# Optimization experiments

Measured on AMD Instinct MI355X. Metric: run time of the kernel, lower is better.

Reference implementation:

```python
import jax, jax.numpy as jnp
import numpy as np

ITERATIONS = 100
TEMP = 1.0
EPS = 0.001


def setup_inputs() -> dict:
    key = jax.random.key(0)
    x = jax.random.normal(key, (16, 512, 512), dtype=jnp.float32)
    return {"x": x}


def reference(x):
    # exp(x / temp) + eps, then 100 alternating row/col normalizations
    y = jnp.exp(x / TEMP) + EPS

    def step(y, _):
        y = y / jnp.sum(y, axis=-1, keepdims=True)  # row normalize
        y = y / jnp.sum(y, axis=-2, keepdims=True)  # column normalize
        return y, None

    y, _ = jax.lax.scan(step, y, None, length=ITERATIONS)
    return y
```

## Files before the change

kernel.cpp:

```cpp
#include <hip/hip_runtime.h>
#include <hip/hip_bf16.h>


#define BATCH   16
#define NDIM    512
#define NNEL    (NDIM * NDIM)
#define ITERS   100
#define EPS_K   0.001f
#define WPB     16
#define RPW     32
#define THREADS 512
#define CSTRIDE 64

__device__ __forceinline__ unsigned short f2bf(float f) {
  unsigned int u = __float_as_uint(f);
  u += 0x7fffu + ((u >> 16) & 1u);
  return (unsigned short)(u >> 16);
}

__global__ __launch_bounds__(256) void prep_kernel(const float* __restrict__ x,
                                                   unsigned short* __restrict__ mh,
                                                   unsigned short* __restrict__ mht,
                                                   int* __restrict__ counters) {
  __shared__ float t[64][65];
  const int bid = blockIdx.x;
  if (bid == 0 && threadIdx.x < 32) counters[(int)threadIdx.x * CSTRIDE] = 0;
  const int b    = bid >> 6;
  const int tile = bid & 63;
  const int tr   = (tile >> 3) << 6;
  const int tc   = (tile & 7) << 6;
  const int lx   = threadIdx.x & 63;
  const int ty   = threadIdx.x >> 6;
  const size_t base = (size_t)b * NNEL;
#pragma unroll
  for (int k = 0; k < 16; ++k) {
    int row = (k << 2) + ty;
    float v = expf(x[base + (size_t)(tr + row) * NDIM + tc + lx]) + EPS_K;
    mh[base + (size_t)(tr + row) * NDIM + tc + lx] = f2bf(v);
    t[row][lx] = v;
  }
  __syncthreads();
#pragma unroll
  for (int k = 0; k < 16; ++k) {
    int row = (k << 2) + ty;
    mht[base + (size_t)(tc + row) * NDIM + tr + lx] = f2bf(t[lx][row]);
  }
}

__device__ __forceinline__ void wg_barrier(int* cnt, int target) {
  __syncthreads();
  if (threadIdx.x == 0) {
    __hip_atomic_fetch_add(cnt, 1, __ATOMIC_RELEASE, __HIP_MEMORY_SCOPE_AGENT);
    int guard = 0;
    while (__hip_atomic_load(cnt, __ATOMIC_RELAXED, __HIP_MEMORY_SCOPE_AGENT) < target) {
      __builtin_amdgcn_s_sleep(2);
      if (++guard > (1 << 22)) break;
    }
    asm volatile("" ::: "memory");
  }
  __syncthreads();
}

__device__ __forceinline__ float dot_row(const unsigned short* mrow, int lane,
                                         const float* cc) {
  uint4 v = *(const uint4*)(mrow + lane * 8);
  float p;
  p  = __uint_as_float(v.x << 16)         * cc[0];
  p += __uint_as_float(v.x & 0xffff0000u) * cc[1];
  p += __uint_as_float(v.y << 16)         * cc[2];
  p += __uint_as_float(v.y & 0xffff0000u) * cc[3];
  p += __uint_as_float(v.z << 16)         * cc[4];
  p += __uint_as_float(v.z & 0xffff0000u) * cc[5];
  p += __uint_as_float(v.w << 16)         * cc[6];
  p += __uint_as_float(v.w & 0xffff0000u) * cc[7];
#pragma unroll
  for (int o = 32; o > 0; o >>= 1) p += __shfl_xor(p, o, 64);
  return p;
}

__global__ __launch_bounds__(THREADS, 4) void sinkhorn_kernel(
    const unsigned short* mh, const unsigned short* mht, float* yout,
    float* r_g, float* c_g, int* counters) {
  __shared__ alignas(16) float vec[NDIM];
  __shared__ float rown[RPW];
  __shared__ alignas(16) unsigned short stage[RPW * NDIM];
  const int wg   = blockIdx.x;
  const int b    = wg >> 4;
  const int sub  = wg & 15;
  const int i0   = sub * RPW;
  const int tid  = threadIdx.x;
  const int w    = tid >> 6;
  const int lane = tid & 63;
  int* bcnt = counters + b * CSTRIDE;
  int* gcnt = counters + 16 * CSTRIDE;
  const size_t mbase = (size_t)b * NNEL;
  float* rg = r_g + b * NDIM;
  float* cg = c_g + b * NDIM;
  int bar = 0;
  float cc[8];
#pragma unroll
  for (int k = 0; k < 8; ++k) cc[k] = 1.0f;

#pragma unroll 1
  for (int t = 0; t < ITERS; ++t) {
    if (t > 0) {
      vec[tid] = __hip_atomic_load(&cg[tid], __ATOMIC_RELAXED, __HIP_MEMORY_SCOPE_AGENT);
      __syncthreads();
      float4 a = ((const float4*)vec)[lane * 2];
      float4 d = ((const float4*)vec)[lane * 2 + 1];
      cc[0] = a.x; cc[1] = a.y; cc[2] = a.z; cc[3] = a.w;
      cc[4] = d.x; cc[5] = d.y; cc[6] = d.z; cc[7] = d.w;
    }
#pragma unroll
    for (int rr = 0; rr < 4; ++rr) {
      int rel = (w << 2) + rr;
      int row = i0 + rel;
      float s = dot_row(mh + mbase + (size_t)row * NDIM, lane, cc);
      if (lane == 0) {
        float rv = 1.0f / s;
        rown[rel] = rv;
        __hip_atomic_store(&rg[row], rv, __ATOMIC_RELAXED, __HIP_MEMORY_SCOPE_AGENT);
      }
    }
    ++bar; wg_barrier(bcnt, WPB * bar);

    vec[tid] = __hip_atomic_load(&rg[tid], __ATOMIC_RELAXED, __HIP_MEMORY_SCOPE_AGENT);
    __syncthreads();
    {
      float4 a = ((const float4*)vec)[lane * 2];
      float4 d = ((const float4*)vec)[lane * 2 + 1];
      cc[0] = a.x; cc[1] = a.y; cc[2] = a.z; cc[3] = a.w;
      cc[4] = d.x; cc[5] = d.y; cc[6] = d.z; cc[7] = d.w;
    }
#pragma unroll
    for (int rr = 0; rr < 4; ++rr) {
      int rel = (w << 2) + rr;
      int col = i0 + rel;
      float s = dot_row(mht + mbase + (size_t)col * NDIM, lane, cc);
      if (lane == 0) {
        __hip_atomic_store(&cg[col], 1.0f / s, __ATOMIC_RELAXED, __HIP_MEMORY_SCOPE_AGENT);
      }
    }
    ++bar; wg_barrier(bcnt, WPB * bar);
  }

  vec[tid] = __hip_atomic_load(&cg[tid], __ATOMIC_RELAXED, __HIP_MEMORY_SCOPE_AGENT);
  const uint4* src = (const uint4*)(mh + mbase + (size_t)i0 * NDIM);
  uint4* dst = (uint4*)stage;
#pragma unroll
  for (int k = 0; k < 4; ++k) dst[tid + k * THREADS] = src[tid + k * THREADS];
  wg_barrier(gcnt, 256);
#pragma unroll
  for (int rr = 0; rr < 4; ++rr) {
    int rel = (w << 2) + rr;
    int row = i0 + rel;
    float rv = rown[rel];
    uint2 ma = *(const uint2*)(stage + rel * NDIM + lane * 4);
    uint2 mb = *(const uint2*)(stage + rel * NDIM + 256 + lane * 4);
    float4 ca = ((const float4*)vec)[lane];
    float4 cb = ((const float4*)(vec + 256))[lane];
    float4 oa, ob;
    oa.x = rv * __uint_as_float(ma.x << 16)         * ca.x;
    oa.y = rv * __uint_as_float(ma.x & 0xffff0000u) * ca.y;
    oa.z = rv * __uint_as_float(ma.y << 16)         * ca.z;
    oa.w = rv * __uint_as_float(ma.y & 0xffff0000u) * ca.w;
    ob.x = rv * __uint_as_float(mb.x << 16)         * cb.x;
    ob.y = rv * __uint_as_float(mb.x & 0xffff0000u) * cb.y;
    ob.z = rv * __uint_as_float(mb.y << 16)         * cb.z;
    ob.w = rv * __uint_as_float(mb.y & 0xffff0000u) * cb.w;
    *(float4*)(yout + mbase + (size_t)row * NDIM + lane * 4) = oa;
    *(float4*)(yout + mbase + (size_t)row * NDIM + 256 + lane * 4) = ob;
  }
}

extern "C" void kernel_launch(void* const* d_in, const int* in_sizes, int n_in,
                              void* d_out, int out_size, void* d_ws, size_t ws_size,
                              hipStream_t stream) {
  const float* x = (const float*)d_in[0];
  float* yout = (float*)d_out;
  unsigned short* mh  = (unsigned short*)d_out;
  unsigned short* mht = mh + (size_t)BATCH * NNEL;
  float* r_g = (float*)d_ws;
  float* c_g = r_g + BATCH * NDIM;
  int* counters = (int*)(c_g + BATCH * NDIM);

  hipLaunchKernelGGL(prep_kernel, dim3(BATCH * 64), dim3(256), 0, stream,
                     x, mh, mht, counters);
  hipLaunchKernelGGL(sinkhorn_kernel, dim3(BATCH * WPB), dim3(THREADS), 0, stream,
                     mh, mht, yout, r_g, c_g, counters);
}
```

Measured before the change: 1.321 ms.

## Replace per-batch atomic barriers with double-buffered tag-based dataflow polling

Drops the two counter-based workgroup barriers per Sinkhorn iteration. Each workgroup now publishes its row and column scale vectors together with a per-producer tag, into double-buffered slots indexed by iteration parity. Consumers' waves spin with `__all` on the tags covering the 8 entries they need, then load the values directly into registers, skipping the LDS broadcast and `__syncthreads`. This is meant to remove the sleep-based barrier latency and serialization, at the cost of busy polling traffic and reliance on tag values that persist across launches.

```diff
diff --git a/kernel.cpp b/kernel.cpp
--- a/kernel.cpp
+++ b/kernel.cpp
@@ -11,6 +11,7 @@
 #define RPW     32
 #define THREADS 512
 #define CSTRIDE 64
+#define TAGS    16
 
 __device__ __forceinline__ unsigned short f2bf(float f) {
   unsigned int u = __float_as_uint(f);
@@ -78,10 +79,57 @@
   return p;
 }
 
+__device__ __forceinline__ void poll_gather8(const int* tags, const float* vals,
+                                             int want, int lane, float* cc) {
+  const int* tp = tags + (lane >> 2);
+  int guard = 0;
+  for (;;) {
+    int tg = __hip_atomic_load(tp, __ATOMIC_RELAXED, __HIP_MEMORY_SCOPE_AGENT);
+    if (__all(tg == want)) break;
+    if (++guard > (1 << 22)) break;
+  }
+  const unsigned long long* vp = (const unsigned long long*)(vals + lane * 8);
+#pragma unroll
+  for (int k = 0; k < 4; ++k) {
+    unsigned long long d =
+        __hip_atomic_load(vp + k, __ATOMIC_RELAXED, __HIP_MEMORY_SCOPE_AGENT);
+    cc[2 * k]     = __uint_as_float((unsigned int)(d & 0xffffffffu));
+    cc[2 * k + 1] = __uint_as_float((unsigned int)(d >> 32));
+  }
+}
+
+__device__ __forceinline__ void poll_gather44(const int* tags, const float* vals,
+                                              int want, int p0, int p1,
+                                              float* a, float* bb) {
+  const int* t0 = tags + (p0 >> 5);
+  const int* t1 = tags + (p1 >> 5);
+  int guard = 0;
+  for (;;) {
+    int g0 = __hip_atomic_load(t0, __ATOMIC_RELAXED, __HIP_MEMORY_SCOPE_AGENT);
+    int g1 = __hip_atomic_load(t1, __ATOMIC_RELAXED, __HIP_MEMORY_SCOPE_AGENT);
+    if (__all((g0 == want) && (g1 == want))) break;
+    if (++guard > (1 << 22)) break;
+  }
+  const unsigned long long* v0 = (const unsigned long long*)(vals + p0);
+  const unsigned long long* v1 = (const unsigned long long*)(vals + p1);
+  unsigned long long d0 = __hip_atomic_load(v0,     __ATOMIC_RELAXED, __HIP_MEMORY_SCOPE_AGENT);
+  unsigned long long d1 = __hip_atomic_load(v0 + 1, __ATOMIC_RELAXED, __HIP_MEMORY_SCOPE_AGENT);
+  unsigned long long d2 = __hip_atomic_load(v1,     __ATOMIC_RELAXED, __HIP_MEMORY_SCOPE_AGENT);
+  unsigned long long d3 = __hip_atomic_load(v1 + 1, __ATOMIC_RELAXED, __HIP_MEMORY_SCOPE_AGENT);
+  a[0]  = __uint_as_float((unsigned int)(d0 & 0xffffffffu));
+  a[1]  = __uint_as_float((unsigned int)(d0 >> 32));
+  a[2]  = __uint_as_float((unsigned int)(d1 & 0xffffffffu));
+  a[3]  = __uint_as_float((unsigned int)(d1 >> 32));
+  bb[0] = __uint_as_float((unsigned int)(d2 & 0xffffffffu));
+  bb[1] = __uint_as_float((unsigned int)(d2 >> 32));
+  bb[2] = __uint_as_float((unsigned int)(d3 & 0xffffffffu));
+  bb[3] = __uint_as_float((unsigned int)(d3 >> 32));
+}
+
 __global__ __launch_bounds__(THREADS, 4) void sinkhorn_kernel(
-    const unsigned short* mh, const unsigned short* mht, float* yout,
-    float* r_g, float* c_g, int* counters) {
-  __shared__ alignas(16) float vec[NDIM];
+    const unsigned short* __restrict__ mh, const unsigned short* __restrict__ mht,
+    float* __restrict__ yout,
+    int* rtag, int* ctag, float* rval, float* cval, int* counters) {
   __shared__ float rown[RPW];
   __shared__ alignas(16) unsigned short stage[RPW * NDIM];
   const int wg   = blockIdx.x;
@@ -91,64 +139,73 @@
   const int tid  = threadIdx.x;
   const int w    = tid >> 6;
   const int lane = tid & 63;
-  int* bcnt = counters + b * CSTRIDE;
   int* gcnt = counters + 16 * CSTRIDE;
   const size_t mbase = (size_t)b * NNEL;
-  float* rg = r_g + b * NDIM;
-  float* cg = c_g + b * NDIM;
-  int bar = 0;
   float cc[8];
 #pragma unroll
   for (int k = 0; k < 8; ++k) cc[k] = 1.0f;
 
 #pragma unroll 1
   for (int t = 0; t < ITERS; ++t) {
+    const int slot  = t & 1;
+    const int pslot = slot ^ 1;
     if (t > 0) {
-      vec[tid] = __hip_atomic_load(&cg[tid], __ATOMIC_RELAXED, __HIP_MEMORY_SCOPE_AGENT);
-      __syncthreads();
-      float4 a = ((const float4*)vec)[lane * 2];
-      float4 d = ((const float4*)vec)[lane * 2 + 1];
-      cc[0] = a.x; cc[1] = a.y; cc[2] = a.z; cc[3] = a.w;
-      cc[4] = d.x; cc[5] = d.y; cc[6] = d.z; cc[7] = d.w;
-    }
+      poll_gather8(ctag + (pslot * BATCH + b) * TAGS,
+                   cval + (pslot * BATCH + b) * NDIM, t, lane, cc);
+    }
+    float rv[4];
 #pragma unroll
     for (int rr = 0; rr < 4; ++rr) {
-      int rel = (w << 2) + rr;
-      int row = i0 + rel;
+      int row = i0 + (w << 2) + rr;
       float s = dot_row(mh + mbase + (size_t)row * NDIM, lane, cc);
-      if (lane == 0) {
-        float rv = 1.0f / s;
-        rown[rel] = rv;
-        __hip_atomic_store(&rg[row], rv, __ATOMIC_RELAXED, __HIP_MEMORY_SCOPE_AGENT);
+      rv[rr] = 1.0f / s;
+    }
+    if (lane == 0) {
+      float* dst = rval + (slot * BATCH + b) * NDIM + i0 + (w << 2);
+#pragma unroll
+      for (int rr = 0; rr < 4; ++rr)
+        __hip_atomic_store(dst + rr, rv[rr], __ATOMIC_RELAXED, __HIP_MEMORY_SCOPE_AGENT);
+      if (t == ITERS - 1) {
+#pragma unroll
+        for (int rr = 0; rr < 4; ++rr) rown[(w << 2) + rr] = rv[rr];
       }
     }
-    ++bar; wg_barrier(bcnt, WPB * bar);
-
-    vec[tid] = __hip_atomic_load(&rg[tid], __ATOMIC_RELAXED, __HIP_MEMORY_SCOPE_AGENT);
     __syncthreads();
-    {
-      float4 a = ((const float4*)vec)[lane * 2];
-      float4 d = ((const float4*)vec)[lane * 2 + 1];
-      cc[0] = a.x; cc[1] = a.y; cc[2] = a.z; cc[3] = a.w;
-      cc[4] = d.x; cc[5] = d.y; cc[6] = d.z; cc[7] = d.w;
-    }
+    if (tid == 0) {
+      __hip_atomic_store(rtag + (slot * BATCH + b) * TAGS + sub, t + 1,
+                         __ATOMIC_RELEASE, __HIP_MEMORY_SCOPE_AGENT);
+    }
+    poll_gather8(rtag + (slot * BATCH + b) * TAGS,
+                 rval + (slot * BATCH + b) * NDIM, t + 1, lane, cc);
+    float cv[4];
 #pragma unroll
     for (int rr = 0; rr < 4; ++rr) {
-      int rel = (w << 2) + rr;
-      int col = i0 + rel;
+      int col = i0 + (w << 2) + rr;
       float s = dot_row(mht + mbase + (size_t)col * NDIM, lane, cc);
-      if (lane == 0) {
-        __hip_atomic_store(&cg[col], 1.0f / s, __ATOMIC_RELAXED, __HIP_MEMORY_SCOPE_AGENT);
-      }
-    }
-    ++bar; wg_barrier(bcnt, WPB * bar);
-  }
-
-  vec[tid] = __hip_atomic_load(&cg[tid], __ATOMIC_RELAXED, __HIP_MEMORY_SCOPE_AGENT);
+      cv[rr] = 1.0f / s;
+    }
+    if (lane == 0) {
+      float* dst = cval + (slot * BATCH + b) * NDIM + i0 + (w << 2);
+#pragma unroll
+      for (int rr = 0; rr < 4; ++rr)
+        __hip_atomic_store(dst + rr, cv[rr], __ATOMIC_RELAXED, __HIP_MEMORY_SCOPE_AGENT);
+    }
+    __syncthreads();
+    if (tid == 0) {
+      __hip_atomic_store(ctag + (slot * BATCH + b) * TAGS + sub, t + 1,
+                         __ATOMIC_RELEASE, __HIP_MEMORY_SCOPE_AGENT);
+    }
+  }
+
   const uint4* src = (const uint4*)(mh + mbase + (size_t)i0 * NDIM);
   uint4* dst = (uint4*)stage;
 #pragma unroll
   for (int k = 0; k < 4; ++k) dst[tid + k * THREADS] = src[tid + k * THREADS];
+  const int fslot = (ITERS - 1) & 1;
+  float ca[4], cb[4];
+  poll_gather44(ctag + (fslot * BATCH + b) * TAGS,
+                cval + (fslot * BATCH + b) * NDIM, ITERS,
+                lane * 4, 256 + lane * 4, ca, cb);
   wg_barrier(gcnt, 256);
 #pragma unroll
   for (int rr = 0; rr < 4; ++rr) {
@@ -157,17 +214,15 @@
     float rv = rown[rel];
     uint2 ma = *(const uint2*)(stage + rel * NDIM + lane * 4);
     uint2 mb = *(const uint2*)(stage + rel * NDIM + 256 + lane * 4);
-    float4 ca = ((const float4*)vec)[lane];
-    float4 cb = ((const float4*)(vec + 256))[lane];
     float4 oa, ob;
-    oa.x = rv * __uint_as_float(ma.x << 16)         * ca.x;
-    oa.y = rv * __uint_as_float(ma.x & 0xffff0000u) * ca.y;
-    oa.z = rv * __uint_as_float(ma.y << 16)         * ca.z;
-    oa.w = rv * __uint_as_float(ma.y & 0xffff0000u) * ca.w;
-    ob.x = rv * __uint_as_float(mb.x << 16)         * cb.x;
-    ob.y = rv * __uint_as_float(mb.x & 0xffff0000u) * cb.y;
-    ob.z = rv * __uint_as_float(mb.y << 16)         * cb.z;
-    ob.w = rv * __uint_as_float(mb.y & 0xffff0000u) * cb.w;
+    oa.x = rv * __uint_as_float(ma.x << 16)         * ca[0];
+    oa.y = rv * __uint_as_float(ma.x & 0xffff0000u) * ca[1];
+    oa.z = rv * __uint_as_float(ma.y << 16)         * ca[2];
+    oa.w = rv * __uint_as_float(ma.y & 0xffff0000u) * ca[3];
+    ob.x = rv * __uint_as_float(mb.x << 16)         * cb[0];
+    ob.y = rv * __uint_as_float(mb.x & 0xffff0000u) * cb[1];
+    ob.z = rv * __uint_as_float(mb.y << 16)         * cb[2];
+    ob.w = rv * __uint_as_float(mb.y & 0xffff0000u) * cb[3];
     *(float4*)(yout + mbase + (size_t)row * NDIM + lane * 4) = oa;
     *(float4*)(yout + mbase + (size_t)row * NDIM + 256 + lane * 4) = ob;
   }
@@ -180,12 +235,14 @@
   float* yout = (float*)d_out;
   unsigned short* mh  = (unsigned short*)d_out;
   unsigned short* mht = mh + (size_t)BATCH * NNEL;
-  float* r_g = (float*)d_ws;
-  float* c_g = r_g + BATCH * NDIM;
-  int* counters = (int*)(c_g + BATCH * NDIM);
+  int*   rtag = (int*)d_ws;
+  int*   ctag = rtag + 2 * BATCH * TAGS;
+  float* rval = (float*)(ctag + 2 * BATCH * TAGS);
+  float* cval = rval + 2 * BATCH * NDIM;
+  int*   counters = (int*)(cval + 2 * BATCH * NDIM);
 
   hipLaunchKernelGGL(prep_kernel, dim3(BATCH * 64), dim3(256), 0, stream,
                      x, mh, mht, counters);
   hipLaunchKernelGGL(sinkhorn_kernel, dim3(BATCH * WPB), dim3(THREADS), 0, stream,
-                     mh, mht, yout, r_g, c_g, counters);
-}
+                     mh, mht, yout, rtag, ctag, rval, cval, counters);
+}
```

Result: no change. 1.344 ms (+1.7%).

## Replace counter barriers with tagged double-buffered flag polling on scaling vectors

Applied to the files above, without the earlier changes.

The per-batch atomic-counter barriers and LDS broadcasts are replaced by having each wave store its row/column scale factors with a 2-bit iteration tag packed into the low mantissa bits, into double-buffered global arrays. Each wave then polls the 512-entry vector directly with cache-bypassing loads until every tag matches. This removes two workgroup barriers and the counter round-trips per iteration. In exchange the low two mantissa bits of each scale factor are lost, and wavefronts spin on global memory.

```diff
diff --git a/kernel.cpp b/kernel.cpp
--- a/kernel.cpp
+++ b/kernel.cpp
@@ -12,10 +12,17 @@
 #define THREADS 512
 #define CSTRIDE 64
 
+typedef __attribute__((ext_vector_type(4))) unsigned int u32x4;
+typedef __attribute__((ext_vector_type(4))) float        f32x4;
+
 __device__ __forceinline__ unsigned short f2bf(float f) {
   unsigned int u = __float_as_uint(f);
   u += 0x7fffu + ((u >> 16) & 1u);
   return (unsigned short)(u >> 16);
+}
+
+__device__ __forceinline__ float tagf(float v, unsigned tag) {
+  return __uint_as_float((__float_as_uint(v) & ~3u) | tag);
 }
 
 __global__ __launch_bounds__(256) void prep_kernel(const float* __restrict__ x,
@@ -78,11 +85,58 @@
   return p;
 }
 
+__device__ __forceinline__ void poll8(const float* vp, unsigned want, float* cc) {
+  u32x4 a, b;
+  int guard = 0;
+  for (;;) {
+    asm volatile(
+        "global_load_dwordx4 %0, %2, off sc1\n\t"
+        "global_load_dwordx4 %1, %3, off sc1\n\t"
+        "s_waitcnt vmcnt(0)"
+        : "=&v"(a), "=&v"(b)
+        : "v"(vp), "v"(vp + 4)
+        : "memory");
+    int ok = ((a[0] & 3u) == want) & ((a[1] & 3u) == want) &
+             ((a[2] & 3u) == want) & ((a[3] & 3u) == want) &
+             ((b[0] & 3u) == want) & ((b[1] & 3u) == want) &
+             ((b[2] & 3u) == want) & ((b[3] & 3u) == want);
+    if (__all(ok)) break;
+    if (++guard > (1 << 20)) break;
+    __builtin_amdgcn_s_sleep(1);
+  }
+  cc[0] = __uint_as_float(a[0]); cc[1] = __uint_as_float(a[1]);
+  cc[2] = __uint_as_float(a[2]); cc[3] = __uint_as_float(a[3]);
+  cc[4] = __uint_as_float(b[0]); cc[5] = __uint_as_float(b[1]);
+  cc[6] = __uint_as_float(b[2]); cc[7] = __uint_as_float(b[3]);
+}
+
+__device__ __forceinline__ void poll4(const float* vp, unsigned want, float* cc) {
+  u32x4 a;
+  int guard = 0;
+  for (;;) {
+    asm volatile(
+        "global_load_dwordx4 %0, %1, off sc1\n\t"
+        "s_waitcnt vmcnt(0)"
+        : "=&v"(a) : "v"(vp) : "memory");
+    int ok = ((a[0] & 3u) == want) & ((a[1] & 3u) == want) &
+             ((a[2] & 3u) == want) & ((a[3] & 3u) == want);
+    if (__all(ok)) break;
+    if (++guard > (1 << 20)) break;
+    __builtin_amdgcn_s_sleep(1);
+  }
+  cc[0] = __uint_as_float(a[0]); cc[1] = __uint_as_float(a[1]);
+  cc[2] = __uint_as_float(a[2]); cc[3] = __uint_as_float(a[3]);
+}
+
+__device__ __forceinline__ void store4(float* dst, float x, float y, float z, float w) {
+  f32x4 q; q[0] = x; q[1] = y; q[2] = z; q[3] = w;
+  asm volatile("global_store_dwordx4 %0, %1, off sc1"
+               :: "v"(dst), "v"(q) : "memory");
+}
+
 __global__ __launch_bounds__(THREADS, 4) void sinkhorn_kernel(
-    const unsigned short* mh, const unsigned short* mht, float* yout,
-    float* r_g, float* c_g, int* counters) {
-  __shared__ alignas(16) float vec[NDIM];
-  __shared__ float rown[RPW];
+    const unsigned short* __restrict__ mh, const unsigned short* __restrict__ mht,
+    float* __restrict__ yout, float* rval, float* cval, int* counters) {
   __shared__ alignas(16) unsigned short stage[RPW * NDIM];
   const int wg   = blockIdx.x;
   const int b    = wg >> 4;
@@ -91,83 +145,74 @@
   const int tid  = threadIdx.x;
   const int w    = tid >> 6;
   const int lane = tid & 63;
-  int* bcnt = counters + b * CSTRIDE;
   int* gcnt = counters + 16 * CSTRIDE;
   const size_t mbase = (size_t)b * NNEL;
-  float* rg = r_g + b * NDIM;
-  float* cg = c_g + b * NDIM;
-  int bar = 0;
   float cc[8];
 #pragma unroll
   for (int k = 0; k < 8; ++k) cc[k] = 1.0f;
+  float rfin[4];
 
 #pragma unroll 1
   for (int t = 0; t < ITERS; ++t) {
-    if (t > 0) {
-      vec[tid] = __hip_atomic_load(&cg[tid], __ATOMIC_RELAXED, __HIP_MEMORY_SCOPE_AGENT);
-      __syncthreads();
-      float4 a = ((const float4*)vec)[lane * 2];
-      float4 d = ((const float4*)vec)[lane * 2 + 1];
-      cc[0] = a.x; cc[1] = a.y; cc[2] = a.z; cc[3] = a.w;
-      cc[4] = d.x; cc[5] = d.y; cc[6] = d.z; cc[7] = d.w;
-    }
+    const int slot = t & 1;
+    if (t > 0)
+      poll8(cval + ((t - 1) & 1) * (BATCH * NDIM) + b * NDIM + lane * 8,
+            (unsigned)((t - 1) & 3), cc);
+    float rv[4];
 #pragma unroll
     for (int rr = 0; rr < 4; ++rr) {
-      int rel = (w << 2) + rr;
-      int row = i0 + rel;
-      float s = dot_row(mh + mbase + (size_t)row * NDIM, lane, cc);
-      if (lane == 0) {
-        float rv = 1.0f / s;
-        rown[rel] = rv;
-        __hip_atomic_store(&rg[row], rv, __ATOMIC_RELAXED, __HIP_MEMORY_SCOPE_AGENT);
-      }
-    }
-    ++bar; wg_barrier(bcnt, WPB * bar);
-
-    vec[tid] = __hip_atomic_load(&rg[tid], __ATOMIC_RELAXED, __HIP_MEMORY_SCOPE_AGENT);
-    __syncthreads();
-    {
-      float4 a = ((const float4*)vec)[lane * 2];
-      float4 d = ((const float4*)vec)[lane * 2 + 1];
-      cc[0] = a.x; cc[1] = a.y; cc[2] = a.z; cc[3] = a.w;
-      cc[4] = d.x; cc[5] = d.y; cc[6] = d.z; cc[7] = d.w;
-    }
+      int row = i0 + (w << 2) + rr;
+      rv[rr] = 1.0f / dot_row(mh + mbase + (size_t)row * NDIM, lane, cc);
+    }
+    if (t == ITERS - 1) {
+#pragma unroll
+      for (int rr = 0; rr < 4; ++rr) rfin[rr] = rv[rr];
+    }
+    if (lane == 0)
+      store4(rval + slot * (BATCH * NDIM) + b * NDIM + i0 + (w << 2),
+             tagf(rv[0], t & 3), tagf(rv[1], t & 3),
+             tagf(rv[2], t & 3), tagf(rv[3], t & 3));
+    poll8(rval + slot * (BATCH * NDIM) + b * NDIM + lane * 8,
+          (unsigned)(t & 3), cc);
+    float cv[4];
 #pragma unroll
     for (int rr = 0; rr < 4; ++rr) {
-      int rel = (w << 2) + rr;
-      int col = i0 + rel;
-      float s = dot_row(mht + mbase + (size_t)col * NDIM, lane, cc);
-      if (lane == 0) {
-        __hip_atomic_store(&cg[col], 1.0f / s, __ATOMIC_RELAXED, __HIP_MEMORY_SCOPE_AGENT);
-      }
-    }
-    ++bar; wg_barrier(bcnt, WPB * bar);
-  }
-
-  vec[tid] = __hip_atomic_load(&cg[tid], __ATOMIC_RELAXED, __HIP_MEMORY_SCOPE_AGENT);
+      int col = i0 + (w << 2) + rr;
+      cv[rr] = 1.0f / dot_row(mht + mbase + (size_t)col * NDIM, lane, cc);
+    }
+    if (lane == 0)
+      store4(cval + slot * (BATCH * NDIM) + b * NDIM + i0 + (w << 2),
+             tagf(cv[0], t & 3), tagf(cv[1], t & 3),
+             tagf(cv[2], t & 3), tagf(cv[3], t & 3));
+  }
+
+  __syncthreads();
   const uint4* src = (const uint4*)(mh + mbase + (size_t)i0 * NDIM);
   uint4* dst = (uint4*)stage;
 #pragma unroll
   for (int k = 0; k < 4; ++k) dst[tid + k * THREADS] = src[tid + k * THREADS];
+  float ca[4], cb[4];
+  const int fslot = (ITERS - 1) & 1;
+  const unsigned fwant = (unsigned)((ITERS - 1) & 3);
+  poll4(cval + fslot * (BATCH * NDIM) + b * NDIM + lane * 4, fwant, ca);
+  poll4(cval + fslot * (BATCH * NDIM) + b * NDIM + 256 + lane * 4, fwant, cb);
   wg_barrier(gcnt, 256);
 #pragma unroll
   for (int rr = 0; rr < 4; ++rr) {
     int rel = (w << 2) + rr;
     int row = i0 + rel;
-    float rv = rown[rel];
+    float rv = rfin[rr];
     uint2 ma = *(const uint2*)(stage + rel * NDIM + lane * 4);
     uint2 mb = *(const uint2*)(stage + rel * NDIM + 256 + lane * 4);
-    float4 ca = ((const float4*)vec)[lane];
-    float4 cb = ((const float4*)(vec + 256))[lane];
     float4 oa, ob;
-    oa.x = rv * __uint_as_float(ma.x << 16)         * ca.x;
-    oa.y = rv * __uint_as_float(ma.x & 0xffff0000u) * ca.y;
-    oa.z = rv * __uint_as_float(ma.y << 16)         * ca.z;
-    oa.w = rv * __uint_as_float(ma.y & 0xffff0000u) * ca.w;
-    ob.x = rv * __uint_as_float(mb.x << 16)         * cb.x;
-    ob.y = rv * __uint_as_float(mb.x & 0xffff0000u) * cb.y;
-    ob.z = rv * __uint_as_float(mb.y << 16)         * cb.z;
-    ob.w = rv * __uint_as_float(mb.y & 0xffff0000u) * cb.w;
+    oa.x = rv * __uint_as_float(ma.x << 16)         * ca[0];
+    oa.y = rv * __uint_as_float(ma.x & 0xffff0000u) * ca[1];
+    oa.z = rv * __uint_as_float(ma.y << 16)         * ca[2];
+    oa.w = rv * __uint_as_float(ma.y & 0xffff0000u) * ca[3];
+    ob.x = rv * __uint_as_float(mb.x << 16)         * cb[0];
+    ob.y = rv * __uint_as_float(mb.x & 0xffff0000u) * cb[1];
+    ob.z = rv * __uint_as_float(mb.y << 16)         * cb[2];
+    ob.w = rv * __uint_as_float(mb.y & 0xffff0000u) * cb[3];
     *(float4*)(yout + mbase + (size_t)row * NDIM + lane * 4) = oa;
     *(float4*)(yout + mbase + (size_t)row * NDIM + 256 + lane * 4) = ob;
   }
@@ -180,12 +225,12 @@
   float* yout = (float*)d_out;
   unsigned short* mh  = (unsigned short*)d_out;
   unsigned short* mht = mh + (size_t)BATCH * NNEL;
-  float* r_g = (float*)d_ws;
-  float* c_g = r_g + BATCH * NDIM;
-  int* counters = (int*)(c_g + BATCH * NDIM);
+  float* rval = (float*)d_ws;
+  float* cval = rval + 2 * BATCH * NDIM;
+  int*   counters = (int*)(cval + 2 * BATCH * NDIM);
 
   hipLaunchKernelGGL(prep_kernel, dim3(BATCH * 64), dim3(256), 0, stream,
                      x, mh, mht, counters);
   hipLaunchKernelGGL(sinkhorn_kernel, dim3(BATCH * WPB), dim3(THREADS), 0, stream,
-                     mh, mht, yout, r_g, c_g, counters);
-}
+                     mh, mht, yout, rval, cval, counters);
+}
```

After: 1.234 ms. 1.07x faster.
